# Kernel tuning notes

Hardware: AMD Instinct MI355X
Metric: run time of the kernel (lower is better)

## Reference

```python
import jax, jax.numpy as jnp
import numpy as np

B, OBJ, INP, HID = 8, 128, 64, 256
D = 3 * INP  # concatenated per-object feature dim


def setup_inputs() -> dict:
    key = jax.random.key(0)
    ks = jax.random.split(key, 12)
    s = 0.02
    return {
        "x0": jax.random.normal(ks[0], (B, OBJ, INP), jnp.float32),
        "x1": jax.random.normal(ks[1], (B, OBJ, INP), jnp.float32),
        "x2": jax.random.normal(ks[2], (B, OBJ, INP), jnp.float32),
        # weights stored [in, out] so forward is x @ w + b
        "w_enc": jax.random.normal(ks[3], (2 * D, HID), jnp.float32) * s,
        "b_enc": jnp.zeros((HID,), jnp.float32),
        "w1": jax.random.normal(ks[4], (HID, HID), jnp.float32) * s,
        "b1": jnp.zeros((HID,), jnp.float32),
        "w2": jax.random.normal(ks[5], (HID, HID), jnp.float32) * s,
        "b2": jnp.zeros((HID,), jnp.float32),
        "w3": jax.random.normal(ks[6], (HID, HID), jnp.float32) * s,
        "b3": jnp.zeros((HID,), jnp.float32),
        "wd1": jax.random.normal(ks[7], (HID, HID), jnp.float32) * s,
        "bd1": jnp.zeros((HID,), jnp.float32),
        "wd2": jax.random.normal(ks[8], (HID, INP), jnp.float32) * s,
        "bd2": jnp.zeros((INP,), jnp.float32),
    }


def reference(x0, x1, x2, w_enc, b_enc, w1, b1, w2, b2, w3, b3, wd1, bd1, wd2, bd2):
    x = jnp.concatenate([x0, x1, x2], axis=-1)  # [B, N, D]
    # Fused equivalent of Linear(cat(e1, e2)): split w_enc rows into the part
    # acting on the first-object features and the second-object features, then
    # broadcast-add instead of materializing the [B,N,N,2D] concat tensor.
    ea = jnp.einsum("bnd,dh->bnh", x, w_enc[:D])   # acts on data_e1
    eb = jnp.einsum("bnd,dh->bnh", x, w_enc[D:])   # acts on data_e2
    h = jax.nn.relu(ea[:, :, None, :] + eb[:, None, :, :] + b_enc)  # [B,N,N,H]
    h = jax.nn.relu(h @ w1 + b1)
    h = jax.nn.relu(h @ w2 + b2)
    h = h @ w3 + b3              # fc3 has no activation before the mean
    pooled = h.mean(axis=2)      # [B, N, H]
    out = jax.nn.relu(pooled @ wd1 + bd1) @ wd2 + bd2  # [B, N, INP]
    return out
```

## Files before the change

### kernel.cpp

```cpp
#include <hip/hip_runtime.h>
#include <stdint.h>


#define HID 256
#define NOBJ 128
#define NROW 1024

typedef __attribute__((ext_vector_type(8))) short short8;
typedef __attribute__((ext_vector_type(4))) float float4v;
typedef __attribute__((ext_vector_type(16))) float float16v;
typedef __attribute__((ext_vector_type(2))) unsigned int uint2v;

__device__ __forceinline__ unsigned int f2bf_u(float f) {
    unsigned int u = __builtin_bit_cast(unsigned int, f);
    u += 0x7fffu + ((u >> 16) & 1u);
    return u >> 16;
}
__device__ __forceinline__ unsigned int pack2(float a, float b) {
    return f2bf_u(a) | (f2bf_u(b) << 16);
}
__device__ __forceinline__ float relu(float v) { return v > 0.f ? v : 0.f; }

__device__ __forceinline__ void lds_barrier() {
    asm volatile("s_waitcnt lgkmcnt(0)\n\ts_barrier" ::: "memory");
}

__global__ void setup_kernel(const float* __restrict__ x0, const float* __restrict__ x1,
                             const float* __restrict__ x2, const float* __restrict__ w_enc,
                             const float* __restrict__ b_enc,
                             const float* __restrict__ w1, const float* __restrict__ w2,
                             const float* __restrict__ w3, const float* __restrict__ b3,
                             const float* __restrict__ wd1, const float* __restrict__ bd1,
                             unsigned short* __restrict__ wt,
                             float* __restrict__ ea, float* __restrict__ eb,
                             float* __restrict__ W34, float* __restrict__ b34,
                             float* __restrict__ msg) {
    const int bx = blockIdx.x, t = threadIdx.x;
    __shared__ float lw[256][33];
    __shared__ float xs[2][192];
    if (bx < 16) {
        const int m = bx >> 3, tau = bx & 7;
        const float* w = (m == 0) ? w1 : w2;
        const int n = t & 31, kk = t >> 5;
#pragma unroll
        for (int rep = 0; rep < 32; ++rep) {
            int k = rep * 8 + kk;
            lw[k][n] = w[k * 256 + tau * 32 + n];
        }
        __syncthreads();
        unsigned short* outp = wt + (m * 8 + tau) * 8192;
        const int lane = t & 63, wq = t >> 6;
        const int h5 = lane >> 5, l31n = lane & 31;
#pragma unroll
        for (int rep = 0; rep < 4; ++rep) {
            const int kb = wq * 4 + rep;
            short8 v;
#pragma unroll
            for (int e = 0; e < 8; ++e)
                v[e] = (short)f2bf_u(lw[kb * 16 + h5 * 8 + e][l31n]);
            *(short8*)(outp + kb * 512 + lane * 8) = v;
        }
        return;
    }
    if (bx < 528) {
        const int e = bx - 16;
        msg[e * 512 + t] = 0.f;
        msg[e * 512 + 256 + t] = 0.f;
        for (int idx = t; idx < 384; idx += 256) {
            int r = idx / 192, d = idx % 192;
            int row = e * 2 + r;
            float v = (d < 64) ? x0[row * 64 + d]
                    : (d < 128) ? x1[row * 64 + d - 64]
                    : x2[row * 64 + d - 128];
            xs[r][d] = v;
        }
        __syncthreads();
        float aA[2] = {0.f, 0.f}, aB[2] = {0.f, 0.f};
#pragma unroll 16
        for (int d = 0; d < 192; ++d) {
            float wa = w_enc[d * 256 + t];
            float wb = w_enc[(192 + d) * 256 + t];
#pragma unroll
            for (int r = 0; r < 2; ++r) { aA[r] += xs[r][d] * wa; aB[r] += xs[r][d] * wb; }
        }
        float be = b_enc[t];
#pragma unroll
        for (int r = 0; r < 2; ++r) {
            ea[(e * 2 + r) * 256 + t] = aA[r] + be;
            eb[(e * 2 + r) * 256 + t] = aB[r];
        }
        return;
    }
    if (bx < 784) {
        const int m = bx - 528;
        float a = 0.f;
#pragma unroll 8
        for (int k = 0; k < 256; ++k) a += w3[m * 256 + k] * wd1[k * 256 + t];
        W34[m * 256 + t] = a;
        return;
    }
    {
        float a = bd1[t];
#pragma unroll 8
        for (int k = 0; k < 256; ++k) a += b3[k] * wd1[k * 256 + t];
        b34[t] = a;
    }
}

__global__ __launch_bounds__(256, 2) void pair_kernel(
        const float* __restrict__ ea, const float* __restrict__ eb,
        const unsigned short* __restrict__ wt,
        const float* __restrict__ b1, const float* __restrict__ b2,
        float* __restrict__ msg) {
    __shared__ __align__(16) unsigned short hbuf[64 * 256];

    const int bx = blockIdx.x;
    const int w = bx >> 1, jh = bx & 1, b = w >> 7;
    const int t = threadIdx.x, wv = t >> 6, lane = t & 63;
    const int l31 = lane & 31, h5 = lane >> 5;
    const int n0 = wv * 64;

    const unsigned short* aptr = wt + lane * 8;

    short8 af[4][2], bfr[2][2];
#pragma unroll
    for (int pg = 0; pg < 3; ++pg) {
        af[pg][0] = *(const short8*)(aptr + ((wv * 2 + 0) * 16 + pg) * 512);
        af[pg][1] = *(const short8*)(aptr + ((wv * 2 + 1) * 16 + pg) * 512);
    }

    {
        const float4v va = *(const float4v*)(ea + w * 256 + lane * 4);
        const float* ebbase = eb + (b * NOBJ + jh * 64) * 256;
        const int c = lane >> 1, sub = (lane & 1) * 4;
#pragma unroll 4
        for (int jj = 0; jj < 16; ++jj) {
            const int j = wv * 16 + jj;
            float4v vb = *(const float4v*)(ebbase + j * 256 + lane * 4);
            int addr = j * 256 + ((c ^ (j & 31)) << 3) + sub;
            *(uint2v*)(hbuf + addr) = (uint2v){
                pack2(relu(va[0] + vb[0]), relu(va[1] + vb[1])),
                pack2(relu(va[2] + vb[2]), relu(va[3] + vb[3]))};
        }
    }
    lds_barrier();

    int jb[2];
#pragma unroll
    for (int tj = 0; tj < 2; ++tj) jb[tj] = (tj * 32 + l31) * 256;
#pragma unroll
    for (int tj = 0; tj < 2; ++tj)
        bfr[0][tj] = *(const short8*)(hbuf + jb[tj] + ((h5 ^ l31) << 3));

    float16v acc[2][2];

#pragma unroll
    for (int l = 0; l < 2; ++l) {
        const float* bias = (l == 0) ? b1 : b2;
#pragma unroll
        for (int tn = 0; tn < 2; ++tn)
#pragma unroll
            for (int q = 0; q < 4; ++q) {
                float4v bv = *(const float4v*)(bias + n0 + tn * 32 + q * 8 + h5 * 4);
#pragma unroll
                for (int i = 0; i < 4; ++i)
#pragma unroll
                    for (int tj = 0; tj < 2; ++tj)
                        acc[tn][tj][q * 4 + i] = bv[i];
            }
#pragma unroll
        for (int kb = 0; kb < 16; ++kb) {
            const int g = l * 16 + kb, gp = g + 3;
            if (gp < 32) {
                const int lp = gp >> 4, kp = gp & 15;
                af[gp & 3][0] = *(const short8*)(aptr + ((lp * 8 + wv * 2 + 0) * 16 + kp) * 512);
                af[gp & 3][1] = *(const short8*)(aptr + ((lp * 8 + wv * 2 + 1) * 16 + kp) * 512);
            }
            if (kb < 15) {
                const int off = ((((kb + 1) * 2 + h5) ^ l31) << 3);
#pragma unroll
                for (int tj = 0; tj < 2; ++tj)
                    bfr[(kb + 1) & 1][tj] = *(const short8*)(hbuf + jb[tj] + off);
            }
#pragma unroll
            for (int tn = 0; tn < 2; ++tn)
#pragma unroll
                for (int tj = 0; tj < 2; ++tj)
                    acc[tn][tj] = __builtin_amdgcn_mfma_f32_32x32x16_bf16(
                        af[g & 3][tn], bfr[kb & 1][tj], acc[tn][tj], 0, 0, 0);
        }

        if (l == 0) {
            lds_barrier();
#pragma unroll
            for (int tn = 0; tn < 2; ++tn)
#pragma unroll
                for (int q = 0; q < 4; ++q) {
                    const int nb_ = n0 + tn * 32 + 8 * q + 4 * h5;
                    const int cn = nb_ >> 3, sub = nb_ & 7;
#pragma unroll
                    for (int tj = 0; tj < 2; ++tj) {
                        const int j = tj * 32 + l31;
                        int addr = j * 256 + ((cn ^ l31) << 3) + sub;
                        *(uint2v*)(hbuf + addr) = (uint2v){
                            pack2(relu(acc[tn][tj][q * 4]), relu(acc[tn][tj][q * 4 + 1])),
                            pack2(relu(acc[tn][tj][q * 4 + 2]), relu(acc[tn][tj][q * 4 + 3]))};
                    }
                }
            lds_barrier();
#pragma unroll
            for (int tj = 0; tj < 2; ++tj)
                bfr[0][tj] = *(const short8*)(hbuf + jb[tj] + ((h5 ^ l31) << 3));
        }
    }

#pragma unroll
    for (int tn = 0; tn < 2; ++tn)
#pragma unroll
        for (int r = 0; r < 16; ++r) {
            float s = relu(acc[tn][0][r]) + relu(acc[tn][1][r]);
            s += __shfl_xor(s, 1);
            s += __shfl_xor(s, 2);
            s += __shfl_xor(s, 4);
            s += __shfl_xor(s, 8);
            s += __shfl_xor(s, 16);
            if (l31 == 0) {
                const int n = n0 + tn * 32 + (r & 3) + 8 * (r >> 2) + 4 * h5;
                atomicAdd(&msg[w * 256 + n], s * 0.0078125f);
            }
        }
}

__global__ __launch_bounds__(512) void decoder_kernel(
        const float* __restrict__ msg, const float* __restrict__ W34,
        const float* __restrict__ b34, const float* __restrict__ wd2,
        const float* __restrict__ bd2, float* __restrict__ out) {
    __shared__ float ml[4][256];
    __shared__ float ps[2][4][256];
    __shared__ float tl[4][256];
    __shared__ float p2[2][4][64];
    const int bx = blockIdx.x, t = threadIdx.x;
    const int r0 = bx * 4;

#pragma unroll
    for (int i = t; i < 1024; i += 512) ml[i >> 8][i & 255] = msg[r0 * 256 + i];
    __syncthreads();

    {
        const int n = t & 255, kh = t >> 8;
        float a0 = 0.f, a1 = 0.f, a2 = 0.f, a3 = 0.f;
        const float* wp = W34 + (kh * 128) * 256 + n;
        const float* m0 = &ml[0][kh * 128];
        const float* m1 = &ml[1][kh * 128];
        const float* m2r = &ml[2][kh * 128];
        const float* m3 = &ml[3][kh * 128];
#pragma unroll 16
        for (int k = 0; k < 128; ++k) {
            const float wv_ = wp[k * 256];
            a0 += m0[k] * wv_;
            a1 += m1[k] * wv_;
            a2 += m2r[k] * wv_;
            a3 += m3[k] * wv_;
        }
        ps[kh][0][n] = a0; ps[kh][1][n] = a1; ps[kh][2][n] = a2; ps[kh][3][n] = a3;
    }
    __syncthreads();
#pragma unroll
    for (int i = t; i < 1024; i += 512) {
        const int r = i >> 8, nn = i & 255;
        tl[r][nn] = relu(ps[0][r][nn] + ps[1][r][nn] + b34[nn]);
    }
    __syncthreads();

    {
        const int o = t & 63, rr = (t >> 6) & 3, kh = t >> 8;
        float a = 0.f;
        const float* w2p = wd2 + (kh * 128) * 64 + o;
        const float* tp = &tl[rr][kh * 128];
#pragma unroll 16
        for (int k = 0; k < 128; ++k) a += tp[k] * w2p[k * 64];
        p2[kh][rr][o] = a;
    }
    __syncthreads();
    if (t < 256) {
        const int o = t & 63, r = t >> 6;
        out[(r0 + r) * 64 + o] = p2[0][r][o] + p2[1][r][o] + bd2[o];
    }
}

extern "C" void kernel_launch(void* const* d_in, const int* in_sizes, int n_in,
                              void* d_out, int out_size, void* d_ws, size_t ws_size,
                              hipStream_t stream) {
    const float* x0    = (const float*)d_in[0];
    const float* x1    = (const float*)d_in[1];
    const float* x2    = (const float*)d_in[2];
    const float* w_enc = (const float*)d_in[3];
    const float* b_enc = (const float*)d_in[4];
    const float* w1    = (const float*)d_in[5];
    const float* b1    = (const float*)d_in[6];
    const float* w2    = (const float*)d_in[7];
    const float* b2    = (const float*)d_in[8];
    const float* w3    = (const float*)d_in[9];
    const float* b3    = (const float*)d_in[10];
    const float* wd1   = (const float*)d_in[11];
    const float* bd1   = (const float*)d_in[12];
    const float* wd2   = (const float*)d_in[13];
    const float* bd2   = (const float*)d_in[14];
    float* out = (float*)d_out;

    unsigned short* wt = (unsigned short*)d_ws;
    float* ea  = (float*)((char*)d_ws + 3 * 65536 * sizeof(unsigned short));
    float* eb  = ea + NROW * HID;
    float* W34 = eb + NROW * HID;
    float* b34 = W34 + 256 * 256;
    float* msg = b34 + 256;

    setup_kernel<<<785, 256, 0, stream>>>(x0, x1, x2, w_enc, b_enc, w1, w2,
                                          w3, b3, wd1, bd1, wt, ea, eb, W34, b34, msg);
    pair_kernel<<<2 * NROW, 256, 0, stream>>>(ea, eb, wt, b1, b2, msg);
    decoder_kernel<<<NROW / 4, 512, 0, stream>>>(msg, W34, b34, wd2, bd2, out);
}
```

Before: 171.1 us.

## Merge j-halves into one 512-thread block and reduce mean in LDS

Each pair block now handles all 128 partner objects with 8 waves, instead of two 256-thread blocks per row. The partial sums are combined in shared memory and written directly, which removes the global atomics and the msg zeroing in setup. It also swaps the manual bf16 packing for the hardware packed-convert instruction, shortens the A-fragment prefetch depth, and raises MFMA wave priority. The shallower prefetch and larger LDS footprint per block may expose more latency.

```diff
diff --git a/kernel.cpp b/kernel.cpp
--- a/kernel.cpp
+++ b/kernel.cpp
@@ -17,7 +17,9 @@
     return u >> 16;
 }
 __device__ __forceinline__ unsigned int pack2(float a, float b) {
-    return f2bf_u(a) | (f2bf_u(b) << 16);
+    unsigned int r;
+    asm("v_cvt_pk_bf16_f32 %0, %1, %2" : "=v"(r) : "v"(a), "v"(b));
+    return r;
 }
 __device__ __forceinline__ float relu(float v) { return v > 0.f ? v : 0.f; }
 
@@ -33,8 +35,7 @@
                              const float* __restrict__ wd1, const float* __restrict__ bd1,
                              unsigned short* __restrict__ wt,
                              float* __restrict__ ea, float* __restrict__ eb,
-                             float* __restrict__ W34, float* __restrict__ b34,
-                             float* __restrict__ msg) {
+                             float* __restrict__ W34, float* __restrict__ b34) {
     const int bx = blockIdx.x, t = threadIdx.x;
     __shared__ float lw[256][33];
     __shared__ float xs[2][192];
@@ -64,8 +65,6 @@
     }
     if (bx < 528) {
         const int e = bx - 16;
-        msg[e * 512 + t] = 0.f;
-        msg[e * 512 + 256 + t] = 0.f;
         for (int idx = t; idx < 384; idx += 256) {
             int r = idx / 192, d = idx % 192;
             int row = e * 2 + r;
@@ -107,31 +106,30 @@
     }
 }
 
-__global__ __launch_bounds__(256, 2) void pair_kernel(
+__global__ __launch_bounds__(512, 4) void pair_kernel(
         const float* __restrict__ ea, const float* __restrict__ eb,
         const unsigned short* __restrict__ wt,
         const float* __restrict__ b1, const float* __restrict__ b2,
         float* __restrict__ msg) {
-    __shared__ __align__(16) unsigned short hbuf[64 * 256];
-
-    const int bx = blockIdx.x;
-    const int w = bx >> 1, jh = bx & 1, b = w >> 7;
+    __shared__ __align__(16) unsigned short hbuf[128 * 256];
+    __shared__ float ms[2][HID];
+
+    const int w = blockIdx.x, b = w >> 7;
     const int t = threadIdx.x, wv = t >> 6, lane = t & 63;
     const int l31 = lane & 31, h5 = lane >> 5;
-    const int n0 = wv * 64;
+    const int nsl = wv & 3, jh = wv >> 2;
+    const int n0 = nsl * 64;
 
     const unsigned short* aptr = wt + lane * 8;
 
-    short8 af[4][2], bfr[2][2];
-#pragma unroll
-    for (int pg = 0; pg < 3; ++pg) {
-        af[pg][0] = *(const short8*)(aptr + ((wv * 2 + 0) * 16 + pg) * 512);
-        af[pg][1] = *(const short8*)(aptr + ((wv * 2 + 1) * 16 + pg) * 512);
-    }
+    short8 af[2][2], bfr[2];
+#pragma unroll
+    for (int tn = 0; tn < 2; ++tn)
+        af[0][tn] = *(const short8*)(aptr + ((nsl * 2 + tn) * 16) * 512);
 
     {
         const float4v va = *(const float4v*)(ea + w * 256 + lane * 4);
-        const float* ebbase = eb + (b * NOBJ + jh * 64) * 256;
+        const float* ebbase = eb + (b * NOBJ) * 256;
         const int c = lane >> 1, sub = (lane & 1) * 4;
 #pragma unroll 4
         for (int jj = 0; jj < 16; ++jj) {
@@ -147,10 +145,7 @@
 
     int jb[2];
 #pragma unroll
-    for (int tj = 0; tj < 2; ++tj) jb[tj] = (tj * 32 + l31) * 256;
-#pragma unroll
-    for (int tj = 0; tj < 2; ++tj)
-        bfr[0][tj] = *(const short8*)(hbuf + jb[tj] + ((h5 ^ l31) << 3));
+    for (int tj = 0; tj < 2; ++tj) jb[tj] = (jh * 64 + tj * 32 + l31) * 256;
 
     float16v acc[2][2];
 
@@ -170,24 +165,28 @@
             }
 #pragma unroll
         for (int kb = 0; kb < 16; ++kb) {
-            const int g = l * 16 + kb, gp = g + 3;
+            const int g = l * 16 + kb, gp = g + 1;
+            {
+                const int off = (((kb * 2 + h5) ^ l31) << 3);
+#pragma unroll
+                for (int tj = 0; tj < 2; ++tj)
+                    bfr[tj] = *(const short8*)(hbuf + jb[tj] + off);
+            }
             if (gp < 32) {
                 const int lp = gp >> 4, kp = gp & 15;
-                af[gp & 3][0] = *(const short8*)(aptr + ((lp * 8 + wv * 2 + 0) * 16 + kp) * 512);
-                af[gp & 3][1] = *(const short8*)(aptr + ((lp * 8 + wv * 2 + 1) * 16 + kp) * 512);
+#pragma unroll
+                for (int tn = 0; tn < 2; ++tn)
+                    af[gp & 1][tn] =
+                        *(const short8*)(aptr + ((lp * 8 + nsl * 2 + tn) * 16 + kp) * 512);
             }
-            if (kb < 15) {
-                const int off = ((((kb + 1) * 2 + h5) ^ l31) << 3);
-#pragma unroll
-                for (int tj = 0; tj < 2; ++tj)
-                    bfr[(kb + 1) & 1][tj] = *(const short8*)(hbuf + jb[tj] + off);
-            }
+            __builtin_amdgcn_s_setprio(1);
 #pragma unroll
             for (int tn = 0; tn < 2; ++tn)
 #pragma unroll
                 for (int tj = 0; tj < 2; ++tj)
                     acc[tn][tj] = __builtin_amdgcn_mfma_f32_32x32x16_bf16(
-                        af[g & 3][tn], bfr[kb & 1][tj], acc[tn][tj], 0, 0, 0);
+                        af[g & 1][tn], bfr[tj], acc[tn][tj], 0, 0, 0);
+            __builtin_amdgcn_s_setprio(0);
         }
 
         if (l == 0) {
@@ -200,7 +199,7 @@
                     const int cn = nb_ >> 3, sub = nb_ & 7;
 #pragma unroll
                     for (int tj = 0; tj < 2; ++tj) {
-                        const int j = tj * 32 + l31;
+                        const int j = jh * 64 + tj * 32 + l31;
                         int addr = j * 256 + ((cn ^ l31) << 3) + sub;
                         *(uint2v*)(hbuf + addr) = (uint2v){
                             pack2(relu(acc[tn][tj][q * 4]), relu(acc[tn][tj][q * 4 + 1])),
@@ -208,9 +207,6 @@
                     }
                 }
             lds_barrier();
-#pragma unroll
-            for (int tj = 0; tj < 2; ++tj)
-                bfr[0][tj] = *(const short8*)(hbuf + jb[tj] + ((h5 ^ l31) << 3));
         }
     }
 
@@ -226,9 +222,18 @@
             s += __shfl_xor(s, 16);
             if (l31 == 0) {
                 const int n = n0 + tn * 32 + (r & 3) + 8 * (r >> 2) + 4 * h5;
-                atomicAdd(&msg[w * 256 + n], s * 0.0078125f);
+                ms[jh][n] = s;
             }
         }
+    __syncthreads();
+    if (t < 64) {
+        const float4v s0 = *(const float4v*)(&ms[0][t * 4]);
+        const float4v s1 = *(const float4v*)(&ms[1][t * 4]);
+        float4v r;
+#pragma unroll
+        for (int i = 0; i < 4; ++i) r[i] = (s0[i] + s1[i]) * 0.0078125f;
+        *(float4v*)(msg + w * 256 + t * 4) = r;
+    }
 }
 
 __global__ __launch_bounds__(512) void decoder_kernel(
@@ -316,7 +321,7 @@
     float* msg = b34 + 256;
 
     setup_kernel<<<785, 256, 0, stream>>>(x0, x1, x2, w_enc, b_enc, w1, w2,
-                                          w3, b3, wd1, bd1, wt, ea, eb, W34, b34, msg);
-    pair_kernel<<<2 * NROW, 256, 0, stream>>>(ea, eb, wt, b1, b2, msg);
+                                          w3, b3, wd1, bd1, wt, ea, eb, W34, b34);
+    pair_kernel<<<NROW, 512, 0, stream>>>(ea, eb, wt, b1, b2, msg);
     decoder_kernel<<<NROW / 4, 512, 0, stream>>>(msg, W34, b34, wd2, bd2, out);
 }
```

Result: faster. 153.9 us (-10.0%).
